# Optimization experiments

Hardware: AMD Instinct MI355X
Metric: run time of the kernel (lower is better)

The kernel has to match this reference:

```python
import jax, jax.numpy as jnp
import numpy as np

B, S, E, H = 4, 2048, 1024, 16
D = E // H  # head_dim = 64


def setup_inputs() -> dict:
    key = jax.random.key(0)
    ks = jax.random.split(key, 5)
    return {
        "hidden_states": jax.random.normal(ks[0], (B, S, E), dtype=jnp.float32),
        "c_attn_w": jax.random.normal(ks[1], (E, 3 * E), dtype=jnp.float32) * 0.02,
        "c_attn_b": jax.random.normal(ks[2], (3 * E,), dtype=jnp.float32) * 0.02,
        "c_proj_w": jax.random.normal(ks[3], (E, E), dtype=jnp.float32) * 0.02,
        "c_proj_b": jax.random.normal(ks[4], (E,), dtype=jnp.float32) * 0.02,
    }


def reference(hidden_states, c_attn_w, c_attn_b, c_proj_w, c_proj_b):
    b, s, e = hidden_states.shape
    # Conv1D c_attn: y = x @ W + b  -> qkv [b, s, 3E]
    qkv = hidden_states @ c_attn_w + c_attn_b
    q, k, v = jnp.split(qkv, 3, axis=-1)
    # split heads -> [b, H, s, D]
    def split_heads(t):
        return t.reshape(b, s, H, D).transpose(0, 2, 1, 3)
    q, k, v = split_heads(q), split_heads(k), split_heads(v)
    # QK^T scaled by sqrt(head_dim)
    scores = jnp.einsum("bhqd,bhkd->bhqk", q, k) / jnp.sqrt(
        jnp.asarray(D, dtype=q.dtype)
    )
    # causal mask (tril), masked positions get dtype min
    causal = jnp.tril(jnp.ones((s, s), dtype=bool))[None, None]
    mask_value = jnp.finfo(scores.dtype).min
    scores = jnp.where(causal, scores, mask_value)
    attn = jax.nn.softmax(scores, axis=-1)
    # attend to values, merge heads
    out = jnp.einsum("bhqk,bhkd->bhqd", attn, v)
    out = out.transpose(0, 2, 1, 3).reshape(b, s, e)
    # Conv1D c_proj
    return out @ c_proj_w + c_proj_b
```

## Files before the change

### kernel.cpp

```cpp
#include <hip/hip_runtime.h>
#include <hip/hip_bf16.h>
#include <cstdint>
#include <cstddef>

#define BB 4
#define SS 2048
#define EE 1024
#define HH 16
#define DD 64

typedef __attribute__((ext_vector_type(8))) short bf16x8;
typedef __attribute__((ext_vector_type(4))) float f32x4;

__device__ __forceinline__ short f2bf(float f) {
    union { float f; uint32_t u; } x; x.f = f;
    uint32_t r = (x.u + 0x7fffu + ((x.u >> 16) & 1u)) >> 16;
    return (short)r;
}
__device__ __forceinline__ short f2bf_fast(float f) {
    union { float f; uint32_t u; } x; x.f = f;
    return (short)((x.u + 0x8000u) >> 16);
}

__device__ __forceinline__ void gload16(const void* g, void* l) {
    __builtin_amdgcn_global_load_lds(
        (__attribute__((address_space(1))) uint32_t*)(uintptr_t)g,
        (__attribute__((address_space(3))) uint32_t*)(uint32_t)(uintptr_t)l,
        16, 0, 0);
}

template<int CTRL>
__device__ __forceinline__ float dppmove(float v) {
    return __int_as_float(__builtin_amdgcn_update_dpp(
        0, __float_as_int(v), CTRL, 0xf, 0xf, true));
}
#define ROW_REDUCE(vals, OP)                                             \
    _Pragma("unroll") for (int _r = 0; _r < 4; ++_r) {                   \
        vals[_r] = OP(vals[_r], dppmove<0xB1>(vals[_r]));                \
        vals[_r] = OP(vals[_r], dppmove<0x4E>(vals[_r]));                \
        vals[_r] = OP(vals[_r], dppmove<0x124>(vals[_r]));               \
        vals[_r] = OP(vals[_r], dppmove<0x128>(vals[_r]));               \
    }
__device__ __forceinline__ float opmax(float a, float b) { return fmaxf(a, b); }
__device__ __forceinline__ float opsum(float a, float b) { return a + b; }

__global__ void cast_kernel(const float* __restrict__ in, short* __restrict__ out, int n4) {
    int stride = gridDim.x * blockDim.x;
    for (int i = blockIdx.x * blockDim.x + threadIdx.x; i < n4; i += stride) {
        float4 v = reinterpret_cast<const float4*>(in)[i];
        short4 o;
        o.x = f2bf(v.x); o.y = f2bf(v.y); o.z = f2bf(v.z); o.w = f2bf(v.w);
        reinterpret_cast<short4*>(out)[i] = o;
    }
}

__global__ void transpose_cast_kernel(const float* __restrict__ in, short* __restrict__ out,
                                      int ncols, int nrows) {
    __shared__ float ts[32][33];
    const int t = threadIdx.x;
    const int r = t >> 3, c4 = (t & 7) * 4;
    const int n0 = blockIdx.x * 32, k0 = blockIdx.y * 32;
    float4 v = *reinterpret_cast<const float4*>(&in[(size_t)(k0 + r) * ncols + n0 + c4]);
    ts[c4 + 0][r] = v.x; ts[c4 + 1][r] = v.y; ts[c4 + 2][r] = v.z; ts[c4 + 3][r] = v.w;
    __syncthreads();
    short4 ov;
    ov.x = f2bf(ts[r][c4 + 0]); ov.y = f2bf(ts[r][c4 + 1]);
    ov.z = f2bf(ts[r][c4 + 2]); ov.w = f2bf(ts[r][c4 + 3]);
    *reinterpret_cast<short4*>(&out[(size_t)(n0 + r) * nrows + k0 + c4]) = ov;
}

__global__ __launch_bounds__(512, 2)
void gemm_qkv(const short* __restrict__ A, const short* __restrict__ Bt,
              const float* __restrict__ bias,
              short* __restrict__ Qo, short* __restrict__ Ko, short* __restrict__ Vo)
{
    __shared__ short As[2][4096];
    __shared__ short Bs[2][8192];
    const int tid  = threadIdx.x;
    const int lane = tid & 63, wid = tid >> 6;
    const int wr = wid >> 2, wc = wid & 3;
    const int l15 = lane & 15, lhi = lane >> 4;
    const int m0 = blockIdx.y * 128, n0 = blockIdx.x * 256;
    const int sr   = lane >> 2;
    const int scol = 8 * ((lane & 3) ^ ((lane >> 3) & 3));
    const int rdx  = (lhi ^ ((l15 >> 1) & 3)) << 4;

    f32x4 acc[4][4] = {};

    gload16(&A[(size_t)(m0 + wid * 16 + sr) * EE + scol], (char*)&As[0][0] + wid * 1024);
    #pragma unroll
    for (int c = 0; c < 2; ++c)
        gload16(&Bt[(size_t)(n0 + wid * 32 + c * 16 + sr) * EE + scol],
                (char*)&Bs[0][0] + wid * 2048 + c * 1024);
    __syncthreads();

    for (int kt = 0; kt < EE / 32; ++kt) {
        const int cur = kt & 1;
        if (kt < EE / 32 - 1) {
            const int kk = (kt + 1) * 32;
            gload16(&A[(size_t)(m0 + wid * 16 + sr) * EE + kk + scol],
                    (char*)&As[cur ^ 1][0] + wid * 1024);
            #pragma unroll
            for (int c = 0; c < 2; ++c)
                gload16(&Bt[(size_t)(n0 + wid * 32 + c * 16 + sr) * EE + kk + scol],
                        (char*)&Bs[cur ^ 1][0] + wid * 2048 + c * 1024);
        }

        bf16x8 af[4], bfr[4];
        #pragma unroll
        for (int mm = 0; mm < 4; ++mm)
            af[mm] = *reinterpret_cast<const bf16x8*>(
                (const char*)&As[cur][0] + (wr * 64 + mm * 16 + l15) * 64 + rdx);
        #pragma unroll
        for (int nn = 0; nn < 4; ++nn)
            bfr[nn] = *reinterpret_cast<const bf16x8*>(
                (const char*)&Bs[cur][0] + (wc * 64 + nn * 16 + l15) * 64 + rdx);
        #pragma unroll
        for (int mm = 0; mm < 4; ++mm)
            #pragma unroll
            for (int nn = 0; nn < 4; ++nn)
                acc[mm][nn] = __builtin_amdgcn_mfma_f32_16x16x32_bf16(af[mm], bfr[nn], acc[mm][nn], 0, 0, 0);

        __syncthreads();
    }

    const int part = n0 >> 10;
    #pragma unroll
    for (int mm = 0; mm < 4; ++mm) {
        #pragma unroll
        for (int nn = 0; nn < 4; ++nn) {
            const int gcol = n0 + wc * 64 + nn * 16 + l15;
            const float bv = bias[gcol];
            const int e = gcol & 1023;
            const int h = e >> 6, d = e & 63;
            const int grow0 = m0 + wr * 64 + mm * 16 + lhi * 4;
            const int bidx = grow0 >> 11;
            const int s0 = grow0 & 2047;
            const int bh = bidx * HH + h;
            if (part == 2) {
                short4 pk;
                pk.x = f2bf(acc[mm][nn][0] + bv);
                pk.y = f2bf(acc[mm][nn][1] + bv);
                pk.z = f2bf(acc[mm][nn][2] + bv);
                pk.w = f2bf(acc[mm][nn][3] + bv);
                *reinterpret_cast<short4*>(&Vo[((size_t)bh * DD + d) * SS + s0]) = pk;
            } else if (part == 0) {
                #pragma unroll
                for (int r = 0; r < 4; ++r)
                    Qo[((size_t)bh * SS + s0 + r) * DD + d] = f2bf((acc[mm][nn][r] + bv) * 0.18033688f);
            } else {
                #pragma unroll
                for (int r = 0; r < 4; ++r)
                    Ko[((size_t)bh * SS + s0 + r) * DD + d] = f2bf(acc[mm][nn][r] + bv);
            }
        }
    }
}

__global__ __launch_bounds__(256, 2)
void gemm_proj(const short* __restrict__ A, const short* __restrict__ Bt,
               const float* __restrict__ bias, float* __restrict__ Co)
{
    __shared__ short As[2][4096];
    __shared__ short Bs[2][4096];
    const int tid  = threadIdx.x;
    const int lane = tid & 63, wid = tid >> 6;
    const int wr = wid >> 1, wc = wid & 1;
    const int l15 = lane & 15, lhi = lane >> 4;
    const int m0 = blockIdx.y * 128, n0 = blockIdx.x * 128;
    const int sr  = lane >> 2;
    const int sc8 = (lane & 3) * 8;

    f32x4 acc[4][4] = {};

    #pragma unroll
    for (int p = 0; p < 2; ++p) {
        const int c = wid * 2 + p;
        gload16(&A [(size_t)(m0 + c * 16 + sr) * EE + sc8], &As[0][c * 512]);
        gload16(&Bt[(size_t)(n0 + c * 16 + sr) * EE + sc8], &Bs[0][c * 512]);
    }
    __syncthreads();

    for (int kt = 0; kt < EE / 32; ++kt) {
        const int cur = kt & 1;
        if (kt < EE / 32 - 1) {
            const int kk = (kt + 1) * 32;
            #pragma unroll
            for (int p = 0; p < 2; ++p) {
                const int c = wid * 2 + p;
                gload16(&A [(size_t)(m0 + c * 16 + sr) * EE + kk + sc8], &As[cur ^ 1][c * 512]);
                gload16(&Bt[(size_t)(n0 + c * 16 + sr) * EE + kk + sc8], &Bs[cur ^ 1][c * 512]);
            }
        }

        bf16x8 af[4], bfr[4];
        #pragma unroll
        for (int mm = 0; mm < 4; ++mm)
            af[mm] = *reinterpret_cast<const bf16x8*>(&As[cur][(wr * 64 + mm * 16 + l15) * 32 + lhi * 8]);
        #pragma unroll
        for (int nn = 0; nn < 4; ++nn)
            bfr[nn] = *reinterpret_cast<const bf16x8*>(&Bs[cur][(wc * 64 + nn * 16 + l15) * 32 + lhi * 8]);
        #pragma unroll
        for (int mm = 0; mm < 4; ++mm)
            #pragma unroll
            for (int nn = 0; nn < 4; ++nn)
                acc[mm][nn] = __builtin_amdgcn_mfma_f32_16x16x32_bf16(af[mm], bfr[nn], acc[mm][nn], 0, 0, 0);

        __syncthreads();
    }

    #pragma unroll
    for (int mm = 0; mm < 4; ++mm) {
        #pragma unroll
        for (int nn = 0; nn < 4; ++nn) {
            const int gcol = n0 + wc * 64 + nn * 16 + l15;
            const float bv = bias[gcol];
            #pragma unroll
            for (int r = 0; r < 4; ++r) {
                const int grow = m0 + wr * 64 + mm * 16 + lhi * 4 + r;
                Co[(size_t)grow * EE + gcol] = acc[mm][nn][r] + bv;
            }
        }
    }
}

__global__ __launch_bounds__(256, 4)
void attn_kernel(const short* __restrict__ Q, const short* __restrict__ K,
                 const short* __restrict__ Vt, short* __restrict__ CTX)
{
    __shared__ short Ks[4096];
    __shared__ short Vs[2][4096];
    __shared__ short Ps[4][1024];
    const int tid  = threadIdx.x;
    const int lane = tid & 63, wid = tid >> 6;
    const int l15 = lane & 15, lhi = lane >> 4;
    const int bid  = blockIdx.x;
    const int bh   = (bid & 7) * 8 + ((bid >> 3) & 7);
    const int pair = bid >> 6;
    const int b = bh >> 4, h = bh & 15;
    const size_t base = (size_t)bh * (SS * DD);
    const short* VtBase = Vt + (size_t)bh * (DD * SS);
    char* const pw = (char*)&Ps[wid][0];

    const int srow = lane >> 3;
    const int scol = 8 * ((lane & 7) ^ srow);

    for (int phase = 0; phase < 2; ++phase) {
        const int t = phase ? (31 - pair) : pair;
        const int q0 = t * 64;
        const int qbase = q0 + wid * 16;

        bf16x8 qa[2];
        qa[0] = *reinterpret_cast<const bf16x8*>(&Q[base + (size_t)(qbase + l15) * DD + lhi * 8]);
        qa[1] = *reinterpret_cast<const bf16x8*>(&Q[base + (size_t)(qbase + l15) * DD + 32 + lhi * 8]);

        f32x4 o[4] = {};
        float lrow[4] = {0.f, 0.f, 0.f, 0.f};

        #pragma unroll
        for (int p = 0; p < 2; ++p) {
            const int c = wid * 2 + p;
            gload16(&K     [base + (size_t)(c * 8 + srow) * DD + scol], (char*)Ks + c * 1024);
            gload16(&VtBase[(size_t)(c * 8 + srow) * SS + scol],        (char*)&Vs[0][0] + c * 1024);
        }
        __syncthreads();

        for (int kt = 0; kt <= t; ++kt) {
            const int cur = kt & 1;

            f32x4 sc[4];
            #pragma unroll
            for (int n = 0; n < 4; ++n) {
                const int row = n * 16 + l15;
                f32x4 cacc = {};
                #pragma unroll
                for (int ks = 0; ks < 2; ++ks) {
                    const int byteoff = (ks * 64 + lhi * 16) ^ ((l15 & 7) << 4);
                    bf16x8 kb = *reinterpret_cast<const bf16x8*>((const char*)Ks + row * 128 + byteoff);
                    cacc = __builtin_amdgcn_mfma_f32_16x16x32_bf16(qa[ks], kb, cacc, 0, 0, 0);
                }
                sc[n] = cacc;
            }

            __syncthreads();

            if (kt < t) {
                const int k1 = (kt + 1) * 64;
                #pragma unroll
                for (int p = 0; p < 2; ++p) {
                    const int c = wid * 2 + p;
                    gload16(&K     [base + (size_t)(k1 + c * 8 + srow) * DD + scol], (char*)Ks + c * 1024);
                    gload16(&VtBase[(size_t)(c * 8 + srow) * SS + k1 + scol], (char*)&Vs[cur ^ 1][0] + c * 1024);
                }
            }

            if (kt == t) {
                #pragma unroll
                for (int n = 0; n < 4; ++n) {
                    const int col = n * 16 + l15;
                    #pragma unroll
                    for (int r = 0; r < 4; ++r) {
                        const int qrow = wid * 16 + lhi * 4 + r;
                        if (col > qrow) sc[n][r] = -1e30f;
                    }
                }
            }
            #pragma unroll
            for (int n = 0; n < 4; ++n)
                #pragma unroll
                for (int r = 0; r < 4; ++r) sc[n][r] = __builtin_amdgcn_exp2f(sc[n][r]);
            #pragma unroll
            for (int n = 0; n < 4; ++n)
                #pragma unroll
                for (int r = 0; r < 4; ++r) {
                    const int q = lhi * 4 + r;
                    const int cb = (n * 32 + l15 * 2) ^ ((q & 7) << 4);
                    *reinterpret_cast<short*>(pw + q * 128 + cb) = f2bf_fast(sc[n][r]);
                }
            bf16x8 pa[2];
            #pragma unroll
            for (int ks = 0; ks < 2; ++ks)
                pa[ks] = *reinterpret_cast<const bf16x8*>(
                    pw + l15 * 128 + ((ks * 64 + lhi * 16) ^ ((l15 & 7) << 4)));
            #pragma unroll
            for (int dg = 0; dg < 4; ++dg) {
                const int row = dg * 16 + l15;
                #pragma unroll
                for (int ks = 0; ks < 2; ++ks) {
                    const int byteoff = (ks * 64 + lhi * 16) ^ ((l15 & 7) << 4);
                    bf16x8 vb = *reinterpret_cast<const bf16x8*>((const char*)&Vs[cur][0] + row * 128 + byteoff);
                    o[dg] = __builtin_amdgcn_mfma_f32_16x16x32_bf16(pa[ks], vb, o[dg], 0, 0, 0);
                }
            }
            float tsum[4];
            #pragma unroll
            for (int r = 0; r < 4; ++r)
                tsum[r] = (sc[0][r] + sc[1][r]) + (sc[2][r] + sc[3][r]);
            ROW_REDUCE(tsum, opsum)
            #pragma unroll
            for (int r = 0; r < 4; ++r) lrow[r] += tsum[r];

            __syncthreads();
        }

        #pragma unroll
        for (int dg = 0; dg < 4; ++dg)
            #pragma unroll
            for (int r = 0; r < 4; ++r) {
                int s = qbase + lhi * 4 + r;
                float val = o[dg][r] / lrow[r];
                CTX[(size_t)(b * SS + s) * EE + h * DD + dg * 16 + l15] = f2bf(val);
            }
    }
}

extern "C" void kernel_launch(void* const* d_in, const int* in_sizes, int n_in,
                              void* d_out, int out_size, void* d_ws, size_t ws_size,
                              hipStream_t stream) {
    const float* hs     = (const float*)d_in[0];
    const float* attn_w = (const float*)d_in[1];
    const float* attn_b = (const float*)d_in[2];
    const float* proj_w = (const float*)d_in[3];
    const float* proj_b = (const float*)d_in[4];
    float* out = (float*)d_out;

    char* ws = (char*)d_ws;
    short* Xb    = (short*)(ws + 0);
    short* WqkvT = (short*)(ws + 16777216);
    short* WprojT= (short*)(ws + 23068672);
    short* Qb    = (short*)(ws + 25165824);
    short* Kb    = (short*)(ws + 41943040);
    short* Vb    = (short*)(ws + 58720256);
    short* CTX   = Xb;

    cast_kernel<<<dim3(2048), dim3(256), 0, stream>>>(hs, Xb, (BB * SS * EE) / 4);
    transpose_cast_kernel<<<dim3(3 * EE / 32, EE / 32), dim3(256), 0, stream>>>(attn_w, WqkvT, 3 * EE, EE);
    transpose_cast_kernel<<<dim3(EE / 32, EE / 32), dim3(256), 0, stream>>>(proj_w, WprojT, EE, EE);

    gemm_qkv<<<dim3(3 * EE / 256, BB * SS / 128), dim3(512), 0, stream>>>(
        Xb, WqkvT, attn_b, Qb, Kb, Vb);

    attn_kernel<<<dim3(1024), dim3(256), 0, stream>>>(Qb, Kb, Vb, CTX);

    gemm_proj<<<dim3(EE / 128, BB * SS / 128), dim3(256), 0, stream>>>(
        CTX, WprojT, proj_b, out);
}
```

Measured before the change: 177.4 us.

## Triple-buffer GEMM LDS tiles with vmcnt-based barriers and swizzle proj loads

```diff
diff --git a/kernel.cpp b/kernel.cpp
--- a/kernel.cpp
+++ b/kernel.cpp
@@ -28,6 +28,11 @@
         (__attribute__((address_space(3))) uint32_t*)(uint32_t)(uintptr_t)l,
         16, 0, 0);
 }
+
+#define WAIT_BARRIER(N)                                          \
+    asm volatile("s_waitcnt vmcnt(" #N ")" ::: "memory");        \
+    __builtin_amdgcn_s_barrier();                                \
+    __builtin_amdgcn_sched_barrier(0);
 
 template<int CTRL>
 __device__ __forceinline__ float dppmove(float v) {
@@ -74,8 +79,8 @@
               const float* __restrict__ bias,
               short* __restrict__ Qo, short* __restrict__ Ko, short* __restrict__ Vo)
 {
-    __shared__ short As[2][4096];
-    __shared__ short Bs[2][8192];
+    __shared__ short As[3][4096];
+    __shared__ short Bs[3][8192];
     const int tid  = threadIdx.x;
     const int lane = tid & 63, wid = tid >> 6;
     const int wr = wid >> 2, wc = wid & 3;
@@ -87,24 +92,24 @@
 
     f32x4 acc[4][4] = {};
 
-    gload16(&A[(size_t)(m0 + wid * 16 + sr) * EE + scol], (char*)&As[0][0] + wid * 1024);
-    #pragma unroll
-    for (int c = 0; c < 2; ++c)
-        gload16(&Bt[(size_t)(n0 + wid * 32 + c * 16 + sr) * EE + scol],
-                (char*)&Bs[0][0] + wid * 2048 + c * 1024);
-    __syncthreads();
-
-    for (int kt = 0; kt < EE / 32; ++kt) {
-        const int cur = kt & 1;
-        if (kt < EE / 32 - 1) {
-            const int kk = (kt + 1) * 32;
-            gload16(&A[(size_t)(m0 + wid * 16 + sr) * EE + kk + scol],
-                    (char*)&As[cur ^ 1][0] + wid * 1024);
-            #pragma unroll
-            for (int c = 0; c < 2; ++c)
-                gload16(&Bt[(size_t)(n0 + wid * 32 + c * 16 + sr) * EE + kk + scol],
-                        (char*)&Bs[cur ^ 1][0] + wid * 2048 + c * 1024);
-        }
+#define QKV_STAGE(tt, bufi)                                                      \
+    {                                                                            \
+        const int kk = (tt) * 32;                                                \
+        gload16(&A[(size_t)(m0 + wid * 16 + sr) * EE + kk + scol],               \
+                (char*)&As[bufi][0] + wid * 1024);                               \
+        gload16(&Bt[(size_t)(n0 + wid * 32 + sr) * EE + kk + scol],              \
+                (char*)&Bs[bufi][0] + wid * 2048);                               \
+        gload16(&Bt[(size_t)(n0 + wid * 32 + 16 + sr) * EE + kk + scol],         \
+                (char*)&Bs[bufi][0] + wid * 2048 + 1024);                        \
+    }
+
+    QKV_STAGE(0, 0)
+    QKV_STAGE(1, 1)
+    WAIT_BARRIER(3)
+
+    for (int kt = 0; kt < 32; ++kt) {
+        const int cur = kt % 3;
+        if (kt + 2 < 32) { const int nb = (kt + 2) % 3; QKV_STAGE(kt + 2, nb) }
 
         bf16x8 af[4], bfr[4];
         #pragma unroll
@@ -121,8 +126,10 @@
             for (int nn = 0; nn < 4; ++nn)
                 acc[mm][nn] = __builtin_amdgcn_mfma_f32_16x16x32_bf16(af[mm], bfr[nn], acc[mm][nn], 0, 0, 0);
 
-        __syncthreads();
-    }
+        if (kt < 30)       { WAIT_BARRIER(3) }
+        else if (kt == 30) { WAIT_BARRIER(0) }
+    }
+#undef QKV_STAGE
 
     const int part = n0 >> 10;
     #pragma unroll
@@ -161,53 +168,59 @@
 void gemm_proj(const short* __restrict__ A, const short* __restrict__ Bt,
                const float* __restrict__ bias, float* __restrict__ Co)
 {
-    __shared__ short As[2][4096];
-    __shared__ short Bs[2][4096];
+    __shared__ short As[3][4096];
+    __shared__ short Bs[3][4096];
     const int tid  = threadIdx.x;
     const int lane = tid & 63, wid = tid >> 6;
     const int wr = wid >> 1, wc = wid & 1;
     const int l15 = lane & 15, lhi = lane >> 4;
     const int m0 = blockIdx.y * 128, n0 = blockIdx.x * 128;
-    const int sr  = lane >> 2;
-    const int sc8 = (lane & 3) * 8;
+    const int sr   = lane >> 2;
+    const int scol = 8 * ((lane & 3) ^ ((lane >> 3) & 3));
+    const int rdx  = (lhi ^ ((l15 >> 1) & 3)) << 4;
 
     f32x4 acc[4][4] = {};
 
-    #pragma unroll
-    for (int p = 0; p < 2; ++p) {
-        const int c = wid * 2 + p;
-        gload16(&A [(size_t)(m0 + c * 16 + sr) * EE + sc8], &As[0][c * 512]);
-        gload16(&Bt[(size_t)(n0 + c * 16 + sr) * EE + sc8], &Bs[0][c * 512]);
-    }
-    __syncthreads();
-
-    for (int kt = 0; kt < EE / 32; ++kt) {
-        const int cur = kt & 1;
-        if (kt < EE / 32 - 1) {
-            const int kk = (kt + 1) * 32;
-            #pragma unroll
-            for (int p = 0; p < 2; ++p) {
-                const int c = wid * 2 + p;
-                gload16(&A [(size_t)(m0 + c * 16 + sr) * EE + kk + sc8], &As[cur ^ 1][c * 512]);
-                gload16(&Bt[(size_t)(n0 + c * 16 + sr) * EE + kk + sc8], &Bs[cur ^ 1][c * 512]);
-            }
-        }
+#define PROJ_STAGE(tt, bufi)                                                     \
+    {                                                                            \
+        const int kk = (tt) * 32;                                                \
+        _Pragma("unroll")                                                        \
+        for (int p = 0; p < 2; ++p) {                                            \
+            const int c = wid * 2 + p;                                           \
+            gload16(&A [(size_t)(m0 + c * 16 + sr) * EE + kk + scol],            \
+                    (char*)&As[bufi][0] + c * 1024);                             \
+            gload16(&Bt[(size_t)(n0 + c * 16 + sr) * EE + kk + scol],            \
+                    (char*)&Bs[bufi][0] + c * 1024);                             \
+        }                                                                        \
+    }
+
+    PROJ_STAGE(0, 0)
+    PROJ_STAGE(1, 1)
+    WAIT_BARRIER(4)
+
+    for (int kt = 0; kt < 32; ++kt) {
+        const int cur = kt % 3;
+        if (kt + 2 < 32) { const int nb = (kt + 2) % 3; PROJ_STAGE(kt + 2, nb) }
 
         bf16x8 af[4], bfr[4];
         #pragma unroll
         for (int mm = 0; mm < 4; ++mm)
-            af[mm] = *reinterpret_cast<const bf16x8*>(&As[cur][(wr * 64 + mm * 16 + l15) * 32 + lhi * 8]);
+            af[mm] = *reinterpret_cast<const bf16x8*>(
+                (const char*)&As[cur][0] + (wr * 64 + mm * 16 + l15) * 64 + rdx);
         #pragma unroll
         for (int nn = 0; nn < 4; ++nn)
-            bfr[nn] = *reinterpret_cast<const bf16x8*>(&Bs[cur][(wc * 64 + nn * 16 + l15) * 32 + lhi * 8]);
+            bfr[nn] = *reinterpret_cast<const bf16x8*>(
+                (const char*)&Bs[cur][0] + (wc * 64 + nn * 16 + l15) * 64 + rdx);
         #pragma unroll
         for (int mm = 0; mm < 4; ++mm)
             #pragma unroll
             for (int nn = 0; nn < 4; ++nn)
                 acc[mm][nn] = __builtin_amdgcn_mfma_f32_16x16x32_bf16(af[mm], bfr[nn], acc[mm][nn], 0, 0, 0);
 
-        __syncthreads();
-    }
+        if (kt < 30)       { WAIT_BARRIER(4) }
+        else if (kt == 30) { WAIT_BARRIER(0) }
+    }
+#undef PROJ_STAGE
 
     #pragma unroll
     for (int mm = 0; mm < 4; ++mm) {
```

After: 169.5 us. 1.05x faster.
